# Kernel optimization log

Hardware: AMD Instinct MI355X
Metric: run time of the kernel (lower is better)

Reference implementation:

```python
import jax, jax.numpy as jnp
import numpy as np

B, LQ, LV, D = 16, 2048, 2048, 1024


def setup_inputs() -> dict:
    key = jax.random.key(0)
    kq, kv = jax.random.split(key)
    query = jax.random.normal(kq, (B, LQ, D), dtype=jnp.float32)
    value = jax.random.normal(kv, (B, LV, D), dtype=jnp.float32)
    return {"query": query, "value": value}


def reference(query, value):
    # score: [B, Lq, Lv] -- unscaled dot-product attention (no 1/sqrt(d))
    score = jnp.einsum('bqd,bvd->bqv', query, value)
    attn = jax.nn.softmax(score, axis=-1)
    # dropout is identity in eval mode
    context = jnp.einsum('bqv,bvd->bqd', attn, value)
    return context
```

## Files before the change

kernel.cpp:

```cpp
#include <hip/hip_runtime.h>


#define B_ 16
#define LQ_ 2048
#define LV_ 2048
#define DD_ 1024

typedef unsigned short u16;
typedef _Float16 f16x8 __attribute__((ext_vector_type(8)));
typedef __attribute__((ext_vector_type(4))) float f32x4;
typedef __attribute__((ext_vector_type(4))) unsigned short u16x4;

__device__ __forceinline__ u16 f2h(float x) {
  union { _Float16 h; u16 u; } c;
  c.h = (_Float16)x;
  return c.u;
}

__device__ __forceinline__ void gload16(const u16* g, u16* lds) {
  __builtin_amdgcn_global_load_lds(
      (const __attribute__((address_space(1))) void*)g,
      (__attribute__((address_space(3))) void*)lds, 16, 0, 0);
}

#define BARRIER() do { asm volatile("" ::: "memory"); __builtin_amdgcn_s_barrier(); asm volatile("" ::: "memory"); } while (0)
#define WAITVM(N) asm volatile("s_waitcnt vmcnt(" #N ")" ::: "memory")

template <int NSEG, int TPS>
__global__ __launch_bounds__(512, 2) void k_gemm8(
    const u16* __restrict__ A0, const u16* __restrict__ B0,
    const u16* __restrict__ A1, const u16* __restrict__ B1,
    float* __restrict__ C, int M, int N, int lda, int ldb,
    size_t aBatch, size_t bBatch) {
  constexpr int NT = NSEG * TPS;
  __shared__ u16 lds[65536];
  u16* ldsA = lds;
  u16* ldsB = lds + 32768;

  int bx, by, bz;
  {
    const int gx = gridDim.x, gy = gridDim.y;
    const int lid = blockIdx.x + gx * (blockIdx.y + gy * blockIdx.z);
    const int nwg = gx * gy * gridDim.z;
    const int q = nwg >> 3;
    const int nid = (lid & 7) * q + (lid >> 3);
    bx = nid % gx;
    const int rem = nid / gx;
    by = rem % gy;
    bz = rem / gy;
  }

  const int tid = threadIdx.x;
  const int w = tid >> 6, l = tid & 63;
  const int m0 = by << 8, n0 = bx << 8;
  const int wr = w >> 2, wc = w & 3;
  const int wr128 = wr * 128, wc64 = wc * 64;
  const int fr = l & 15, kx = l >> 4, fr7 = l & 7;
  const int srow = l >> 3;
  const int gsrc8 = (((l & 7) ^ ((l >> 3) & 7)) << 3);

  const u16* sA0 = A0 + (size_t)bz * aBatch;
  const u16* sB0 = B0 + (size_t)bz * bBatch;
  const u16* sA1 = A1 + (size_t)bz * aBatch;
  const u16* sB1 = B1 + (size_t)bz * bBatch;
  float* Cb = C + (size_t)bz * M * N;

#define PICKAB(tt, Ap_, Bp_)                          \
  const u16 *Ap_ = sA0, *Bp_ = sB0;                   \
  if (NSEG > 1 && (tt) / TPS == 1) { Ap_ = sA1; Bp_ = sB1; }

#define STAGE_A(tt, h)                                                          \
  do {                                                                          \
    PICKAB(tt, Ap_, Bp_); (void)Bp_;                                            \
    const int kk_ = ((tt) % TPS) * 64;                                          \
    u16* d0_ = ldsA + ((tt) & 1) * 16384 + ((h) * 64 + w * 8) * 64;             \
    const u16* g0_ = Ap_ + (size_t)(m0 + (h) * 64 + w * 8 + srow) * lda + kk_ + gsrc8; \
    gload16(g0_, d0_);                                                          \
    gload16(g0_ + (size_t)128 * lda, d0_ + 128 * 64);                           \
  } while (0)

#define STAGE_B(tt, h)                                                          \
  do {                                                                          \
    PICKAB(tt, Ap_, Bp_); (void)Ap_;                                            \
    const int kk_ = ((tt) % TPS) * 64;                                          \
    const int rb_ = (w >> 2) * 64 + (h) * 32 + (w & 3) * 8;                     \
    u16* d0_ = ldsB + ((tt) & 1) * 16384 + rb_ * 64;                            \
    const u16* g0_ = Bp_ + (size_t)(n0 + rb_ + srow) * ldb + kk_ + gsrc8;       \
    gload16(g0_, d0_);                                                          \
    gload16(g0_ + (size_t)128 * ldb, d0_ + 128 * 64);                           \
  } while (0)

#define RA8(MOFF)                                                                   \
  {                                                                                 \
    _Pragma("unroll") for (int m_ = 0; m_ < 4; ++m_) {                              \
      _Pragma("unroll") for (int k_ = 0; k_ < 2; ++k_) {                            \
        af[m_][k_] = *(const f16x8*)(ldsA + bufo +                                  \
            (wr128 + (MOFF) + m_ * 16 + fr) * 64 + (((kx + k_ * 4) ^ fr7) << 3));   \
      }                                                                             \
    }                                                                               \
  }

#define RB4(NF0)                                                                    \
  {                                                                                 \
    _Pragma("unroll") for (int n_ = 0; n_ < 2; ++n_) {                              \
      _Pragma("unroll") for (int k_ = 0; k_ < 2; ++k_) {                            \
        bf[(NF0) + n_][k_] = *(const f16x8*)(ldsB + bufo +                          \
            (wc64 + ((NF0) + n_) * 16 + fr) * 64 + (((kx + k_ * 4) ^ fr7) << 3));   \
      }                                                                             \
    }                                                                               \
  }

#define MFMA8(MF0, NF0)                                                             \
  {                                                                                 \
    _Pragma("unroll") for (int m_ = 0; m_ < 4; ++m_)                                \
    _Pragma("unroll") for (int n_ = 0; n_ < 2; ++n_)                                \
    _Pragma("unroll") for (int k_ = 0; k_ < 2; ++k_)                                \
        acc[(MF0) + m_][(NF0) + n_] = __builtin_amdgcn_mfma_f32_16x16x32_f16(       \
            af[m_][k_], bf[(NF0) + n_][k_], acc[(MF0) + m_][(NF0) + n_], 0, 0, 0);  \
  }

  f32x4 acc[8][4];
#pragma unroll
  for (int i = 0; i < 8; ++i)
#pragma unroll
    for (int j = 0; j < 4; ++j) acc[i][j] = (f32x4){0.f, 0.f, 0.f, 0.f};
  f16x8 af[4][2], bf[4][2];

  STAGE_A(0, 0); STAGE_A(0, 1); STAGE_B(0, 0); STAGE_B(0, 1);
  STAGE_A(1, 0); STAGE_B(1, 0); STAGE_A(1, 1);
  WAITVM(6);
  BARRIER();

#pragma unroll 2
  for (int t = 0; t < NT; ++t) {
    const int bufo = (t & 1) * 16384;
    RA8(0);
    RB4(0);
    if (t + 1 < NT) STAGE_B(t + 1, 1);
    BARRIER();
    __builtin_amdgcn_s_setprio(1); MFMA8(0, 0); __builtin_amdgcn_s_setprio(0);
    BARRIER();
    RB4(2);
    if (t + 2 < NT) STAGE_A(t + 2, 0);
    BARRIER();
    __builtin_amdgcn_s_setprio(1); MFMA8(0, 2); __builtin_amdgcn_s_setprio(0);
    BARRIER();
    RA8(64);
    if (t + 2 < NT) STAGE_B(t + 2, 0);
    BARRIER();
    __builtin_amdgcn_s_setprio(1); MFMA8(4, 0); __builtin_amdgcn_s_setprio(0);
    BARRIER();
    if (t + 2 < NT) STAGE_A(t + 2, 1);
    BARRIER();
    __builtin_amdgcn_s_setprio(1); MFMA8(4, 2); __builtin_amdgcn_s_setprio(0);
    if (t + 2 < NT) { WAITVM(6); } else if (t + 1 < NT) { WAITVM(0); }
    BARRIER();
  }

  const int crow = (l >> 4) * 4;
  const int ccol = l & 15;
#pragma unroll
  for (int mf = 0; mf < 8; ++mf)
#pragma unroll
    for (int nf = 0; nf < 4; ++nf) {
      float* cp = Cb + (size_t)(m0 + wr128 + mf * 16 + crow) * N + (n0 + wc64 + nf * 16 + ccol);
#pragma unroll
      for (int j = 0; j < 4; ++j) cp[(size_t)j * N] = acc[mf][nf][j];
    }
#undef PICKAB
#undef STAGE_A
#undef STAGE_B
#undef RA8
#undef RB4
#undef MFMA8
}

__global__ __launch_bounds__(256) void k_conv_q(const float* __restrict__ in,
                                                u16* __restrict__ hi_o, int nrows) {
  int t = blockIdx.x * 256 + threadIdx.x;
  int total = nrows * (DD_ / 4);
  if (t >= total) return;
  int row = t >> 8;
  int c4 = (t & 255) << 2;
  float4 v = *(const float4*)(in + (size_t)row * DD_ + c4);
  u16x4 hi;
  hi.x = f2h(v.x);
  hi.y = f2h(v.y);
  hi.z = f2h(v.z);
  hi.w = f2h(v.w);
  *(u16x4*)(hi_o + (size_t)row * DD_ + c4) = hi;
}

__global__ __launch_bounds__(256) void k_conv_vt(const float* __restrict__ V,
                                                 u16* __restrict__ Vh,
                                                 u16* __restrict__ VT) {
  __shared__ u16 tile[64][65];
  const int d0 = blockIdx.x * 64, v0 = blockIdx.y * 64;
  const size_t boff = (size_t)blockIdx.z * LV_ * DD_;
  const float* Vb = V + boff;
  u16* Vhb = Vh + boff;
  u16* VTb = VT + (size_t)blockIdx.z * DD_ * LV_;
  const int t = threadIdx.x;
  const int r = t >> 4, c4 = (t & 15) * 4;
#pragma unroll
  for (int i = 0; i < 4; ++i) {
    int row = r + i * 16;
    float4 x = *(const float4*)(Vb + (size_t)(v0 + row) * DD_ + d0 + c4);
    u16x4 h;
    h.x = f2h(x.x);
    h.y = f2h(x.y);
    h.z = f2h(x.z);
    h.w = f2h(x.w);
    *(u16x4*)(Vhb + (size_t)(v0 + row) * DD_ + d0 + c4) = h;
    tile[row][c4 + 0] = h.x;
    tile[row][c4 + 1] = h.y;
    tile[row][c4 + 2] = h.z;
    tile[row][c4 + 3] = h.w;
  }
  __syncthreads();
#pragma unroll
  for (int i = 0; i < 4; ++i) {
    int row = r + i * 16;
    u16x4 o;
    o.x = tile[c4 + 0][row];
    o.y = tile[c4 + 1][row];
    o.z = tile[c4 + 2][row];
    o.w = tile[c4 + 3][row];
    *(u16x4*)(VTb + (size_t)(d0 + row) * LV_ + v0 + c4) = o;
  }
}

__global__ __launch_bounds__(256) void k_softmax(const float* __restrict__ S,
                                                 u16* __restrict__ P, int nrows) {
  const int w = threadIdx.x >> 6, l = threadIdx.x & 63;
  const int row = blockIdx.x * 4 + w;
  if (row >= nrows) return;
  const float* s = S + (size_t)row * LV_;
  u16* p = P + (size_t)row * LV_;
  float4 v[8];
  float m = -3.0e38f;
#pragma unroll
  for (int i = 0; i < 8; ++i) {
    v[i] = *(const float4*)(s + (l << 2) + (i << 8));
    m = fmaxf(m, fmaxf(fmaxf(v[i].x, v[i].y), fmaxf(v[i].z, v[i].w)));
  }
#pragma unroll
  for (int off = 32; off > 0; off >>= 1) m = fmaxf(m, __shfl_xor(m, off, 64));
  float sum = 0.f;
#pragma unroll
  for (int i = 0; i < 8; ++i) {
    v[i].x = __expf(v[i].x - m);
    v[i].y = __expf(v[i].y - m);
    v[i].z = __expf(v[i].z - m);
    v[i].w = __expf(v[i].w - m);
    sum += v[i].x + v[i].y + v[i].z + v[i].w;
  }
#pragma unroll
  for (int off = 32; off > 0; off >>= 1) sum += __shfl_xor(sum, off, 64);
  const float inv = 1.0f / sum;
#pragma unroll
  for (int i = 0; i < 8; ++i) {
    u16x4 o;
    o.x = f2h(v[i].x * inv);
    o.y = f2h(v[i].y * inv);
    o.z = f2h(v[i].z * inv);
    o.w = f2h(v[i].w * inv);
    *(u16x4*)(p + (l << 2) + (i << 8)) = o;
  }
}

extern "C" void kernel_launch(void* const* d_in, const int* in_sizes, int n_in,
                              void* d_out, int out_size, void* d_ws, size_t ws_size,
                              hipStream_t stream) {
  const float* Q = (const float*)d_in[0];
  const float* V = (const float*)d_in[1];
  float* out = (float*)d_out;

  const size_t qv_e = (size_t)LQ_ * DD_;
  const size_t vt_e = (size_t)DD_ * LV_;
  const size_t s_e = (size_t)LQ_ * LV_;
  const size_t p_e = (size_t)LQ_ * LV_;
  const size_t per_batch = qv_e * 2 * 2 + vt_e * 2 + s_e * 4 + p_e * 2;

  int nb = (int)(ws_size / per_batch);
  if (nb < 1) nb = 1;
  if (nb > B_) nb = B_;

  char* wp = (char*)d_ws;
  u16* Qh = (u16*)wp; wp += (size_t)nb * qv_e * 2;
  u16* Vh = (u16*)wp; wp += (size_t)nb * qv_e * 2;
  u16* VT = (u16*)wp; wp += (size_t)nb * vt_e * 2;
  float* S = (float*)wp; wp += (size_t)nb * s_e * 4;
  u16* P = (u16*)wp;

  for (int b0 = 0; b0 < B_; b0 += nb) {
    const int cb = (nb < B_ - b0) ? nb : (B_ - b0);
    const int rows = cb * LQ_;
    const int cthreads = rows * (DD_ / 4);
    k_conv_q<<<dim3((cthreads + 255) / 256), dim3(256), 0, stream>>>(
        Q + (size_t)b0 * LQ_ * DD_, Qh, rows);
    k_conv_vt<<<dim3(DD_ / 64, LV_ / 64, cb), dim3(256), 0, stream>>>(
        V + (size_t)b0 * LV_ * DD_, Vh, VT);
    k_gemm8<1, 16><<<dim3(LV_ / 256, LQ_ / 256, cb), dim3(512), 0, stream>>>(
        Qh, Vh, Qh, Vh, S, LQ_, LV_, DD_, DD_, qv_e, qv_e);
    k_softmax<<<dim3(rows / 4), dim3(256), 0, stream>>>(S, P, rows);
    k_gemm8<1, 32><<<dim3(DD_ / 256, LQ_ / 256, cb), dim3(512), 0, stream>>>(
        P, VT, P, VT, out + (size_t)b0 * LQ_ * DD_, LQ_, DD_, LV_, LV_, p_e, vt_e);
  }
}
```

Before: 514.2 us.

## Fuse softmax into QK^T GEMM with row-panel online softmax

Replaces the separate QK^T GEMM, fp32 score buffer and softmax kernel with a row-panel kernel. Each workgroup owns 128 query rows, sweeps all value columns in 256-wide chunks, and keeps a running max and sum per row. It writes unnormalized fp16 exponentials per chunk, then rescales its P panel in place at the end. The second GEMM uses the same 128-row panel layout. This removes the fp32 S round-trip and one launch, but the grid shrinks to 16×batch workgroups with 128×256 tiles, which may lower occupancy and parallelism. It also adds a reread and rewrite pass over P.

```diff
diff --git a/kernel.cpp b/kernel.cpp
--- a/kernel.cpp
+++ b/kernel.cpp
@@ -26,153 +26,235 @@
 #define BARRIER() do { asm volatile("" ::: "memory"); __builtin_amdgcn_s_barrier(); asm volatile("" ::: "memory"); } while (0)
 #define WAITVM(N) asm volatile("s_waitcnt vmcnt(" #N ")" ::: "memory")
 
-template <int NSEG, int TPS>
-__global__ __launch_bounds__(512, 2) void k_gemm8(
-    const u16* __restrict__ A0, const u16* __restrict__ B0,
-    const u16* __restrict__ A1, const u16* __restrict__ B1,
-    float* __restrict__ C, int M, int N, int lda, int ldb,
-    size_t aBatch, size_t bBatch) {
-  constexpr int NT = NSEG * TPS;
-  __shared__ u16 lds[65536];
+template <int TPS, int NCHUNK, bool FUSE>
+__global__ __launch_bounds__(512, 2) void k_panel(
+    const u16* __restrict__ A, const u16* __restrict__ B,
+    u16* __restrict__ Pout, float* __restrict__ Fout,
+    int ldA, int ldB, int Ntot,
+    size_t aBatch, size_t bBatch, size_t cBatch) {
+  constexpr int NTOT = TPS * NCHUNK;
+  __shared__ u16 lds[49152];
   u16* ldsA = lds;
-  u16* ldsB = lds + 32768;
-
-  int bx, by, bz;
+  u16* ldsB = lds + 16384;
+  __shared__ float red[4][128];
+  __shared__ float mc_lds[NCHUNK][128];
+  __shared__ float sums[128];
+  __shared__ float ftab[NCHUNK][128];
+
+  int bx, bz;
   {
-    const int gx = gridDim.x, gy = gridDim.y;
-    const int lid = blockIdx.x + gx * (blockIdx.y + gy * blockIdx.z);
-    const int nwg = gx * gy * gridDim.z;
-    const int q = nwg >> 3;
-    const int nid = (lid & 7) * q + (lid >> 3);
-    bx = nid % gx;
-    const int rem = nid / gx;
-    by = rem % gy;
-    bz = rem / gy;
+    const int lid = blockIdx.x + 16 * blockIdx.z;
+    if (gridDim.z == 16) {
+      const int u = lid & 7, v = lid >> 3;
+      bz = u + 8 * (v >> 4);
+      bx = v & 15;
+    } else {
+      bx = blockIdx.x;
+      bz = blockIdx.z;
+    }
   }
 
   const int tid = threadIdx.x;
   const int w = tid >> 6, l = tid & 63;
-  const int m0 = by << 8, n0 = bx << 8;
-  const int wr = w >> 2, wc = w & 3;
-  const int wr128 = wr * 128, wc64 = wc * 64;
-  const int fr = l & 15, kx = l >> 4, fr7 = l & 7;
+  const int m0 = bx << 7;
+  const int wr64 = (w >> 2) * 64, wc64 = (w & 3) * 64;
+  const int fr = l & 15, kx = l >> 4, fr7 = l & 7, cc = l & 15;
   const int srow = l >> 3;
+  const int rg4 = (l >> 4) * 4;
   const int gsrc8 = (((l & 7) ^ ((l >> 3) & 7)) << 3);
 
-  const u16* sA0 = A0 + (size_t)bz * aBatch;
-  const u16* sB0 = B0 + (size_t)bz * bBatch;
-  const u16* sA1 = A1 + (size_t)bz * aBatch;
-  const u16* sB1 = B1 + (size_t)bz * bBatch;
-  float* Cb = C + (size_t)bz * M * N;
-
-#define PICKAB(tt, Ap_, Bp_)                          \
-  const u16 *Ap_ = sA0, *Bp_ = sB0;                   \
-  if (NSEG > 1 && (tt) / TPS == 1) { Ap_ = sA1; Bp_ = sB1; }
-
-#define STAGE_A(tt, h)                                                          \
-  do {                                                                          \
-    PICKAB(tt, Ap_, Bp_); (void)Bp_;                                            \
-    const int kk_ = ((tt) % TPS) * 64;                                          \
-    u16* d0_ = ldsA + ((tt) & 1) * 16384 + ((h) * 64 + w * 8) * 64;             \
-    const u16* g0_ = Ap_ + (size_t)(m0 + (h) * 64 + w * 8 + srow) * lda + kk_ + gsrc8; \
-    gload16(g0_, d0_);                                                          \
-    gload16(g0_ + (size_t)128 * lda, d0_ + 128 * 64);                           \
+  const u16* Ab = A + (size_t)bz * aBatch;
+  const u16* Bb = B + (size_t)bz * bBatch;
+  u16* Pc = FUSE ? (Pout + (size_t)bz * cBatch) : nullptr;
+  float* Fc = FUSE ? nullptr : (Fout + (size_t)bz * cBatch);
+
+#define STAGE_A(gt, h)                                                         \
+  do {                                                                         \
+    const int kk_ = ((gt) % TPS) * 64;                                         \
+    const int ar_ = (w >> 2) * 64 + (h) * 32 + (w & 3) * 8;                    \
+    u16* d_ = ldsA + ((gt) & 1) * 8192 + ar_ * 64;                             \
+    gload16(Ab + (size_t)(m0 + ar_ + srow) * ldA + kk_ + gsrc8, d_);           \
   } while (0)
 
-#define STAGE_B(tt, h)                                                          \
-  do {                                                                          \
-    PICKAB(tt, Ap_, Bp_); (void)Ap_;                                            \
-    const int kk_ = ((tt) % TPS) * 64;                                          \
-    const int rb_ = (w >> 2) * 64 + (h) * 32 + (w & 3) * 8;                     \
-    u16* d0_ = ldsB + ((tt) & 1) * 16384 + rb_ * 64;                            \
-    const u16* g0_ = Bp_ + (size_t)(n0 + rb_ + srow) * ldb + kk_ + gsrc8;       \
-    gload16(g0_, d0_);                                                          \
-    gload16(g0_ + (size_t)128 * ldb, d0_ + 128 * 64);                           \
+#define STAGE_B(gt, h)                                                         \
+  do {                                                                         \
+    const int kk_ = ((gt) % TPS) * 64;                                         \
+    const int n0_ = ((gt) / TPS) * 256;                                        \
+    const int rb_ = (w >> 2) * 64 + (h) * 32 + (w & 3) * 8;                    \
+    u16* d_ = ldsB + ((gt) & 1) * 16384 + rb_ * 64;                            \
+    const u16* g_ = Bb + (size_t)(n0_ + rb_ + srow) * ldB + kk_ + gsrc8;       \
+    gload16(g_, d_);                                                           \
+    gload16(g_ + (size_t)128 * ldB, d_ + 8192);                                \
   } while (0)
 
-#define RA8(MOFF)                                                                   \
-  {                                                                                 \
-    _Pragma("unroll") for (int m_ = 0; m_ < 4; ++m_) {                              \
-      _Pragma("unroll") for (int k_ = 0; k_ < 2; ++k_) {                            \
-        af[m_][k_] = *(const f16x8*)(ldsA + bufo +                                  \
-            (wr128 + (MOFF) + m_ * 16 + fr) * 64 + (((kx + k_ * 4) ^ fr7) << 3));   \
-      }                                                                             \
-    }                                                                               \
-  }
-
-#define RB4(NF0)                                                                    \
-  {                                                                                 \
-    _Pragma("unroll") for (int n_ = 0; n_ < 2; ++n_) {                              \
-      _Pragma("unroll") for (int k_ = 0; k_ < 2; ++k_) {                            \
-        bf[(NF0) + n_][k_] = *(const f16x8*)(ldsB + bufo +                          \
-            (wc64 + ((NF0) + n_) * 16 + fr) * 64 + (((kx + k_ * 4) ^ fr7) << 3));   \
-      }                                                                             \
-    }                                                                               \
-  }
-
-#define MFMA8(MF0, NF0)                                                             \
-  {                                                                                 \
-    _Pragma("unroll") for (int m_ = 0; m_ < 4; ++m_)                                \
-    _Pragma("unroll") for (int n_ = 0; n_ < 2; ++n_)                                \
-    _Pragma("unroll") for (int k_ = 0; k_ < 2; ++k_)                                \
-        acc[(MF0) + m_][(NF0) + n_] = __builtin_amdgcn_mfma_f32_16x16x32_f16(       \
-            af[m_][k_], bf[(NF0) + n_][k_], acc[(MF0) + m_][(NF0) + n_], 0, 0, 0);  \
-  }
-
-  f32x4 acc[8][4];
-#pragma unroll
-  for (int i = 0; i < 8; ++i)
+#define RA2(MH)                                                                \
+  { _Pragma("unroll") for (int m_ = 0; m_ < 2; ++m_)                           \
+    _Pragma("unroll") for (int k_ = 0; k_ < 2; ++k_)                           \
+      af[m_][k_] = *(const f16x8*)(ldsA + bufoA +                              \
+          (wr64 + ((MH) * 2 + m_) * 16 + fr) * 64 +                            \
+          (((kx + k_ * 4) ^ fr7) << 3)); }
+
+#define RB4(NF0)                                                               \
+  { _Pragma("unroll") for (int n_ = 0; n_ < 2; ++n_)                           \
+    _Pragma("unroll") for (int k_ = 0; k_ < 2; ++k_)                           \
+      bf[(NF0) + n_][k_] = *(const f16x8*)(ldsB + bufoB +                      \
+          (wc64 + ((NF0) + n_) * 16 + fr) * 64 +                               \
+          (((kx + k_ * 4) ^ fr7) << 3)); }
+
+#define MFMA4(MH, NF0)                                                         \
+  { _Pragma("unroll") for (int m_ = 0; m_ < 2; ++m_)                           \
+    _Pragma("unroll") for (int n_ = 0; n_ < 2; ++n_)                           \
+    _Pragma("unroll") for (int k_ = 0; k_ < 2; ++k_)                           \
+      acc[(MH) * 2 + m_][(NF0) + n_] = __builtin_amdgcn_mfma_f32_16x16x32_f16( \
+          af[m_][k_], bf[(NF0) + n_][k_], acc[(MH) * 2 + m_][(NF0) + n_],      \
+          0, 0, 0); }
+
+  f32x4 acc[4][4];
+#pragma unroll
+  for (int i = 0; i < 4; ++i)
 #pragma unroll
     for (int j = 0; j < 4; ++j) acc[i][j] = (f32x4){0.f, 0.f, 0.f, 0.f};
-  f16x8 af[4][2], bf[4][2];
+  f16x8 af[2][2], bf[4][2];
+  float m_run[4][4], s_run[4][4];
+#pragma unroll
+  for (int i = 0; i < 4; ++i)
+#pragma unroll
+    for (int j = 0; j < 4; ++j) { m_run[i][j] = -1.0e30f; s_run[i][j] = 0.f; }
 
   STAGE_A(0, 0); STAGE_A(0, 1); STAGE_B(0, 0); STAGE_B(0, 1);
   STAGE_A(1, 0); STAGE_B(1, 0); STAGE_A(1, 1);
-  WAITVM(6);
+  WAITVM(4);
   BARRIER();
 
 #pragma unroll 2
-  for (int t = 0; t < NT; ++t) {
-    const int bufo = (t & 1) * 16384;
-    RA8(0);
-    RB4(0);
-    if (t + 1 < NT) STAGE_B(t + 1, 1);
-    BARRIER();
-    __builtin_amdgcn_s_setprio(1); MFMA8(0, 0); __builtin_amdgcn_s_setprio(0);
+  for (int gt = 0; gt < NTOT; ++gt) {
+    const int bufoA = (gt & 1) * 8192;
+    const int bufoB = (gt & 1) * 16384;
+    RA2(0); RB4(0);
+    if (gt + 1 < NTOT) STAGE_B(gt + 1, 1);
+    BARRIER();
+    __builtin_amdgcn_s_setprio(1); MFMA4(0, 0); __builtin_amdgcn_s_setprio(0);
     BARRIER();
     RB4(2);
-    if (t + 2 < NT) STAGE_A(t + 2, 0);
-    BARRIER();
-    __builtin_amdgcn_s_setprio(1); MFMA8(0, 2); __builtin_amdgcn_s_setprio(0);
-    BARRIER();
-    RA8(64);
-    if (t + 2 < NT) STAGE_B(t + 2, 0);
-    BARRIER();
-    __builtin_amdgcn_s_setprio(1); MFMA8(4, 0); __builtin_amdgcn_s_setprio(0);
-    BARRIER();
-    if (t + 2 < NT) STAGE_A(t + 2, 1);
-    BARRIER();
-    __builtin_amdgcn_s_setprio(1); MFMA8(4, 2); __builtin_amdgcn_s_setprio(0);
-    if (t + 2 < NT) { WAITVM(6); } else if (t + 1 < NT) { WAITVM(0); }
-    BARRIER();
-  }
-
-  const int crow = (l >> 4) * 4;
-  const int ccol = l & 15;
-#pragma unroll
-  for (int mf = 0; mf < 8; ++mf)
-#pragma unroll
-    for (int nf = 0; nf < 4; ++nf) {
-      float* cp = Cb + (size_t)(m0 + wr128 + mf * 16 + crow) * N + (n0 + wc64 + nf * 16 + ccol);
-#pragma unroll
-      for (int j = 0; j < 4; ++j) cp[(size_t)j * N] = acc[mf][nf][j];
-    }
-#undef PICKAB
+    if (gt + 2 < NTOT) STAGE_A(gt + 2, 0);
+    BARRIER();
+    __builtin_amdgcn_s_setprio(1); MFMA4(0, 2); __builtin_amdgcn_s_setprio(0);
+    BARRIER();
+    RA2(1);
+    if (gt + 2 < NTOT) STAGE_B(gt + 2, 0);
+    BARRIER();
+    __builtin_amdgcn_s_setprio(1); MFMA4(1, 0); __builtin_amdgcn_s_setprio(0);
+    BARRIER();
+    if (gt + 2 < NTOT) STAGE_A(gt + 2, 1);
+    BARRIER();
+    __builtin_amdgcn_s_setprio(1); MFMA4(1, 2); __builtin_amdgcn_s_setprio(0);
+    if (gt + 2 < NTOT) { WAITVM(4); } else { WAITVM(0); }
+    BARRIER();
+
+    if ((gt & (TPS - 1)) == (TPS - 1)) {
+      const int c_ = gt / TPS;
+      if constexpr (FUSE) {
+        BARRIER();
+#pragma unroll
+        for (int mf = 0; mf < 4; ++mf)
+#pragma unroll
+          for (int j = 0; j < 4; ++j) {
+            float v = fmaxf(fmaxf(acc[mf][0][j], acc[mf][1][j]),
+                            fmaxf(acc[mf][2][j], acc[mf][3][j]));
+#pragma unroll
+            for (int off = 1; off < 16; off <<= 1)
+              v = fmaxf(v, __shfl_xor(v, off, 64));
+            if ((l & 15) == 0) red[w & 3][wr64 + mf * 16 + rg4 + j] = v;
+          }
+        BARRIER();
+        float csum[4][4], mloc[4][4];
+#pragma unroll
+        for (int mf = 0; mf < 4; ++mf)
+#pragma unroll
+          for (int j = 0; j < 4; ++j) {
+            const int r_ = wr64 + mf * 16 + rg4 + j;
+            const float mc_ = fmaxf(fmaxf(red[0][r_], red[1][r_]),
+                                    fmaxf(red[2][r_], red[3][r_]));
+            const float mnew = fmaxf(m_run[mf][j], mc_);
+            float cs = 0.f;
+#pragma unroll
+            for (int nf = 0; nf < 4; ++nf) {
+              const float e = __expf(acc[mf][nf][j] - mnew);
+              cs += e;
+              Pc[(size_t)(m0 + r_) * 2048 + c_ * 256 + wc64 + nf * 16 + cc] = f2h(e);
+            }
+#pragma unroll
+            for (int off = 1; off < 16; off <<= 1) cs += __shfl_xor(cs, off, 64);
+            csum[mf][j] = cs;
+            mloc[mf][j] = mnew;
+          }
+        BARRIER();
+#pragma unroll
+        for (int mf = 0; mf < 4; ++mf)
+#pragma unroll
+          for (int j = 0; j < 4; ++j)
+            if ((l & 15) == 0) red[w & 3][wr64 + mf * 16 + rg4 + j] = csum[mf][j];
+        BARRIER();
+#pragma unroll
+        for (int mf = 0; mf < 4; ++mf)
+#pragma unroll
+          for (int j = 0; j < 4; ++j) {
+            const int r_ = wr64 + mf * 16 + rg4 + j;
+            const float tot = red[0][r_] + red[1][r_] + red[2][r_] + red[3][r_];
+            s_run[mf][j] = s_run[mf][j] * __expf(m_run[mf][j] - mloc[mf][j]) + tot;
+            m_run[mf][j] = mloc[mf][j];
+            if ((w & 3) == 0 && (l & 15) == 0) mc_lds[c_][r_] = m_run[mf][j];
+          }
+        BARRIER();
+      } else {
+#pragma unroll
+        for (int mf = 0; mf < 4; ++mf)
+#pragma unroll
+          for (int nf = 0; nf < 4; ++nf) {
+            float* cp = Fc + (size_t)(m0 + wr64 + mf * 16 + rg4) * Ntot +
+                        c_ * 256 + wc64 + nf * 16 + cc;
+#pragma unroll
+            for (int j = 0; j < 4; ++j) cp[(size_t)j * Ntot] = acc[mf][nf][j];
+          }
+      }
+#pragma unroll
+      for (int i = 0; i < 4; ++i)
+#pragma unroll
+        for (int j = 0; j < 4; ++j) acc[i][j] = (f32x4){0.f, 0.f, 0.f, 0.f};
+    }
+  }
+
+  if constexpr (FUSE) {
+    WAITVM(0);
+    BARRIER();
+    if ((w & 3) == 0 && (l & 15) == 0) {
+#pragma unroll
+      for (int mf = 0; mf < 4; ++mf)
+#pragma unroll
+        for (int j = 0; j < 4; ++j)
+          sums[wr64 + mf * 16 + rg4 + j] = s_run[mf][j];
+    }
+    BARRIER();
+    for (int i = tid; i < NCHUNK * 128; i += 512) {
+      const int c = i >> 7, r = i & 127;
+      ftab[c][r] = __expf(mc_lds[c][r] - mc_lds[NCHUNK - 1][r]) / sums[r];
+    }
+    BARRIER();
+    for (int i = tid; i < 128 * 256; i += 512) {
+      const int r = i >> 8, cp = i & 255;
+      f16x8* p = (f16x8*)(Pc + (size_t)(m0 + r) * 2048 + cp * 8);
+      f16x8 v = *p;
+      const float f = ftab[cp >> 5][r];
+#pragma unroll
+      for (int e = 0; e < 8; ++e) v[e] = (_Float16)((float)v[e] * f);
+      *p = v;
+    }
+  }
 #undef STAGE_A
 #undef STAGE_B
-#undef RA8
+#undef RA2
 #undef RB4
-#undef MFMA8
+#undef MFMA4
 }
 
 __global__ __launch_bounds__(256) void k_conv_q(const float* __restrict__ in,
@@ -230,45 +312,6 @@
   }
 }
 
-__global__ __launch_bounds__(256) void k_softmax(const float* __restrict__ S,
-                                                 u16* __restrict__ P, int nrows) {
-  const int w = threadIdx.x >> 6, l = threadIdx.x & 63;
-  const int row = blockIdx.x * 4 + w;
-  if (row >= nrows) return;
-  const float* s = S + (size_t)row * LV_;
-  u16* p = P + (size_t)row * LV_;
-  float4 v[8];
-  float m = -3.0e38f;
-#pragma unroll
-  for (int i = 0; i < 8; ++i) {
-    v[i] = *(const float4*)(s + (l << 2) + (i << 8));
-    m = fmaxf(m, fmaxf(fmaxf(v[i].x, v[i].y), fmaxf(v[i].z, v[i].w)));
-  }
-#pragma unroll
-  for (int off = 32; off > 0; off >>= 1) m = fmaxf(m, __shfl_xor(m, off, 64));
-  float sum = 0.f;
-#pragma unroll
-  for (int i = 0; i < 8; ++i) {
-    v[i].x = __expf(v[i].x - m);
-    v[i].y = __expf(v[i].y - m);
-    v[i].z = __expf(v[i].z - m);
-    v[i].w = __expf(v[i].w - m);
-    sum += v[i].x + v[i].y + v[i].z + v[i].w;
-  }
-#pragma unroll
-  for (int off = 32; off > 0; off >>= 1) sum += __shfl_xor(sum, off, 64);
-  const float inv = 1.0f / sum;
-#pragma unroll
-  for (int i = 0; i < 8; ++i) {
-    u16x4 o;
-    o.x = f2h(v[i].x * inv);
-    o.y = f2h(v[i].y * inv);
-    o.z = f2h(v[i].z * inv);
-    o.w = f2h(v[i].w * inv);
-    *(u16x4*)(p + (l << 2) + (i << 8)) = o;
-  }
-}
-
 extern "C" void kernel_launch(void* const* d_in, const int* in_sizes, int n_in,
                               void* d_out, int out_size, void* d_ws, size_t ws_size,
                               hipStream_t stream) {
@@ -278,9 +321,8 @@
 
   const size_t qv_e = (size_t)LQ_ * DD_;
   const size_t vt_e = (size_t)DD_ * LV_;
-  const size_t s_e = (size_t)LQ_ * LV_;
   const size_t p_e = (size_t)LQ_ * LV_;
-  const size_t per_batch = qv_e * 2 * 2 + vt_e * 2 + s_e * 4 + p_e * 2;
+  const size_t per_batch = qv_e * 2 * 2 + vt_e * 2 + p_e * 2;
 
   int nb = (int)(ws_size / per_batch);
   if (nb < 1) nb = 1;
@@ -290,7 +332,6 @@
   u16* Qh = (u16*)wp; wp += (size_t)nb * qv_e * 2;
   u16* Vh = (u16*)wp; wp += (size_t)nb * qv_e * 2;
   u16* VT = (u16*)wp; wp += (size_t)nb * vt_e * 2;
-  float* S = (float*)wp; wp += (size_t)nb * s_e * 4;
   u16* P = (u16*)wp;
 
   for (int b0 = 0; b0 < B_; b0 += nb) {
@@ -301,10 +342,10 @@
         Q + (size_t)b0 * LQ_ * DD_, Qh, rows);
     k_conv_vt<<<dim3(DD_ / 64, LV_ / 64, cb), dim3(256), 0, stream>>>(
         V + (size_t)b0 * LV_ * DD_, Vh, VT);
-    k_gemm8<1, 16><<<dim3(LV_ / 256, LQ_ / 256, cb), dim3(512), 0, stream>>>(
-        Qh, Vh, Qh, Vh, S, LQ_, LV_, DD_, DD_, qv_e, qv_e);
-    k_softmax<<<dim3(rows / 4), dim3(256), 0, stream>>>(S, P, rows);
-    k_gemm8<1, 32><<<dim3(DD_ / 256, LQ_ / 256, cb), dim3(512), 0, stream>>>(
-        P, VT, P, VT, out + (size_t)b0 * LQ_ * DD_, LQ_, DD_, LV_, LV_, p_e, vt_e);
-  }
-}
+    k_panel<16, 8, true><<<dim3(16, 1, cb), dim3(512), 0, stream>>>(
+        Qh, Vh, P, nullptr, DD_, DD_, LV_, qv_e, qv_e, p_e);
+    k_panel<32, 4, false><<<dim3(16, 1, cb), dim3(512), 0, stream>>>(
+        P, VT, nullptr, out + (size_t)b0 * LQ_ * DD_, LV_, LV_, DD_, p_e, vt_e,
+        (size_t)LQ_ * DD_);
+  }
+}
```

Result: slower. 589.5 us (+14.7%).

## Fuse softmax into QK GEMM epilogue with per-tile stats and rescale in PV GEMM

Applied to the files above, without the earlier changes.

Removes the fp32 score buffer and the separate softmax kernel. The first GEMM epilogue now computes tile-local row max, writes unnormalized exp as fp16 and records per-tile max and sum. A small stats kernel combines the eight column-tile partials into per-tile rescale factors and the reciprocal denominator. The PV GEMM scales A fragments by those factors in registers and applies the final normalization on store. This saves the large fp32 write and read of S, at the cost of extra epilogue reductions, LDS use and fp16 multiplies in the inner loop.

```diff
diff --git a/kernel.cpp b/kernel.cpp
--- a/kernel.cpp
+++ b/kernel.cpp
@@ -26,14 +26,18 @@
 #define BARRIER() do { asm volatile("" ::: "memory"); __builtin_amdgcn_s_barrier(); asm volatile("" ::: "memory"); } while (0)
 #define WAITVM(N) asm volatile("s_waitcnt vmcnt(" #N ")" ::: "memory")
 
-template <int NSEG, int TPS>
+template <int TPS, int MODE>
 __global__ __launch_bounds__(512, 2) void k_gemm8(
-    const u16* __restrict__ A0, const u16* __restrict__ B0,
-    const u16* __restrict__ A1, const u16* __restrict__ B1,
-    float* __restrict__ C, int M, int N, int lda, int ldb,
-    size_t aBatch, size_t bBatch) {
-  constexpr int NT = NSEG * TPS;
+    const u16* __restrict__ A, const u16* __restrict__ B,
+    u16* __restrict__ Pout, float* __restrict__ Fout,
+    const u16* __restrict__ r2tab, const float* __restrict__ fintab,
+    float* __restrict__ mtab, float* __restrict__ stab,
+    int N, int lda, int ldb, size_t aBatch, size_t bBatch, size_t cBatch) {
+  constexpr int NT = TPS;
   __shared__ u16 lds[65536];
+  __shared__ float red[4][256];
+  __shared__ u16 ldsR2[2048];
+  __shared__ float ldsFin[256];
   u16* ldsA = lds;
   u16* ldsB = lds + 32768;
 
@@ -55,39 +59,38 @@
   const int m0 = by << 8, n0 = bx << 8;
   const int wr = w >> 2, wc = w & 3;
   const int wr128 = wr * 128, wc64 = wc * 64;
-  const int fr = l & 15, kx = l >> 4, fr7 = l & 7;
+  const int fr = l & 15, kx = l >> 4, fr7 = l & 7, cc = l & 15;
   const int srow = l >> 3;
   const int gsrc8 = (((l & 7) ^ ((l >> 3) & 7)) << 3);
 
-  const u16* sA0 = A0 + (size_t)bz * aBatch;
-  const u16* sB0 = B0 + (size_t)bz * bBatch;
-  const u16* sA1 = A1 + (size_t)bz * aBatch;
-  const u16* sB1 = B1 + (size_t)bz * bBatch;
-  float* Cb = C + (size_t)bz * M * N;
-
-#define PICKAB(tt, Ap_, Bp_)                          \
-  const u16 *Ap_ = sA0, *Bp_ = sB0;                   \
-  if (NSEG > 1 && (tt) / TPS == 1) { Ap_ = sA1; Bp_ = sB1; }
+  const u16* Ab = A + (size_t)bz * aBatch;
+  const u16* Bb = B + (size_t)bz * bBatch;
+
+  if constexpr (MODE == 2) {
+    for (int i = tid; i < 2048; i += 512)
+      ldsR2[i] = r2tab[((size_t)bz * 8 + (i >> 8)) * 2048 + m0 + (i & 255)];
+    for (int i = tid; i < 256; i += 512)
+      ldsFin[i] = fintab[(size_t)bz * 2048 + m0 + i];
+    __syncthreads();
+  }
 
 #define STAGE_A(tt, h)                                                          \
   do {                                                                          \
-    PICKAB(tt, Ap_, Bp_); (void)Bp_;                                            \
-    const int kk_ = ((tt) % TPS) * 64;                                          \
+    const int kk_ = (tt) * 64;                                                  \
     u16* d0_ = ldsA + ((tt) & 1) * 16384 + ((h) * 64 + w * 8) * 64;             \
-    const u16* g0_ = Ap_ + (size_t)(m0 + (h) * 64 + w * 8 + srow) * lda + kk_ + gsrc8; \
+    const u16* g0_ = Ab + (size_t)(m0 + (h) * 64 + w * 8 + srow) * lda + kk_ + gsrc8; \
     gload16(g0_, d0_);                                                          \
     gload16(g0_ + (size_t)128 * lda, d0_ + 128 * 64);                           \
   } while (0)
 
 #define STAGE_B(tt, h)                                                          \
   do {                                                                          \
-    PICKAB(tt, Ap_, Bp_); (void)Ap_;                                            \
-    const int kk_ = ((tt) % TPS) * 64;                                          \
+    const int kk_ = (tt) * 64;                                                  \
     const int rb_ = (w >> 2) * 64 + (h) * 32 + (w & 3) * 8;                     \
     u16* d0_ = ldsB + ((tt) & 1) * 16384 + rb_ * 64;                            \
-    const u16* g0_ = Bp_ + (size_t)(n0 + rb_ + srow) * ldb + kk_ + gsrc8;       \
+    const u16* g0_ = Bb + (size_t)(n0 + rb_ + srow) * ldb + kk_ + gsrc8;        \
     gload16(g0_, d0_);                                                          \
-    gload16(g0_ + (size_t)128 * ldb, d0_ + 128 * 64);                           \
+    gload16(g0_ + (size_t)128 * ldb, d0_ + 8192);                               \
   } while (0)
 
 #define RA8(MOFF)                                                                   \
@@ -96,6 +99,7 @@
       _Pragma("unroll") for (int k_ = 0; k_ < 2; ++k_) {                            \
         af[m_][k_] = *(const f16x8*)(ldsA + bufo +                                  \
             (wr128 + (MOFF) + m_ * 16 + fr) * 64 + (((kx + k_ * 4) ^ fr7) << 3));   \
+        if constexpr (MODE == 2) af[m_][k_] = af[m_][k_] * r2h[(MOFF) / 16 + m_];   \
       }                                                                             \
     }                                                                               \
   }
@@ -125,6 +129,7 @@
 #pragma unroll
     for (int j = 0; j < 4; ++j) acc[i][j] = (f32x4){0.f, 0.f, 0.f, 0.f};
   f16x8 af[4][2], bf[4][2];
+  _Float16 r2h[8];
 
   STAGE_A(0, 0); STAGE_A(0, 1); STAGE_B(0, 0); STAGE_B(0, 1);
   STAGE_A(1, 0); STAGE_B(1, 0); STAGE_A(1, 1);
@@ -134,6 +139,14 @@
 #pragma unroll 2
   for (int t = 0; t < NT; ++t) {
     const int bufo = (t & 1) * 16384;
+    if constexpr (MODE == 2) {
+      if ((t & 3) == 0) {
+        const int chb = (t >> 2) * 256;
+#pragma unroll
+        for (int i = 0; i < 8; ++i)
+          r2h[i] = *(const _Float16*)&ldsR2[chb + wr128 + i * 16 + fr];
+      }
+    }
     RA8(0);
     RB4(0);
     if (t + 1 < NT) STAGE_B(t + 1, 1);
@@ -157,22 +170,97 @@
     BARRIER();
   }
 
-  const int crow = (l >> 4) * 4;
-  const int ccol = l & 15;
-#pragma unroll
-  for (int mf = 0; mf < 8; ++mf)
-#pragma unroll
-    for (int nf = 0; nf < 4; ++nf) {
-      float* cp = Cb + (size_t)(m0 + wr128 + mf * 16 + crow) * N + (n0 + wc64 + nf * 16 + ccol);
-#pragma unroll
-      for (int j = 0; j < 4; ++j) cp[(size_t)j * N] = acc[mf][nf][j];
+  const int rg4 = (l >> 4) * 4;
+  if constexpr (MODE == 1) {
+    float mt[8][4];
+#pragma unroll
+    for (int mf = 0; mf < 8; ++mf)
+#pragma unroll
+      for (int j = 0; j < 4; ++j) {
+        float v = fmaxf(fmaxf(acc[mf][0][j], acc[mf][1][j]),
+                        fmaxf(acc[mf][2][j], acc[mf][3][j]));
+#pragma unroll
+        for (int off = 1; off < 16; off <<= 1) v = fmaxf(v, __shfl_xor(v, off, 64));
+        if ((l & 15) == 0) red[w & 3][wr128 + mf * 16 + rg4 + j] = v;
+      }
+    __syncthreads();
+#pragma unroll
+    for (int mf = 0; mf < 8; ++mf)
+#pragma unroll
+      for (int j = 0; j < 4; ++j) {
+        const int r_ = wr128 + mf * 16 + rg4 + j;
+        mt[mf][j] = fmaxf(fmaxf(red[0][r_], red[1][r_]), fmaxf(red[2][r_], red[3][r_]));
+      }
+    __syncthreads();
+    u16* Pc = Pout + (size_t)bz * ((size_t)2048 * 2048);
+#pragma unroll
+    for (int mf = 0; mf < 8; ++mf)
+#pragma unroll
+      for (int j = 0; j < 4; ++j) {
+        const int r_ = wr128 + mf * 16 + rg4 + j;
+        float s = 0.f;
+#pragma unroll
+        for (int nf = 0; nf < 4; ++nf) {
+          const float e = __expf(acc[mf][nf][j] - mt[mf][j]);
+          s += e;
+          Pc[(size_t)(m0 + r_) * 2048 + n0 + wc64 + nf * 16 + cc] = f2h(e);
+        }
+#pragma unroll
+        for (int off = 1; off < 16; off <<= 1) s += __shfl_xor(s, off, 64);
+        if ((l & 15) == 0) red[w & 3][r_] = s;
+      }
+    __syncthreads();
+    if (((w & 3) == 0) && ((l & 15) == 0)) {
+#pragma unroll
+      for (int mf = 0; mf < 8; ++mf)
+#pragma unroll
+        for (int j = 0; j < 4; ++j) {
+          const int r_ = wr128 + mf * 16 + rg4 + j;
+          const float st = red[0][r_] + red[1][r_] + red[2][r_] + red[3][r_];
+          mtab[((size_t)bz * 8 + bx) * 2048 + m0 + r_] = mt[mf][j];
+          stab[((size_t)bz * 8 + bx) * 2048 + m0 + r_] = st;
+        }
     }
-#undef PICKAB
+  } else {
+#pragma unroll
+    for (int mf = 0; mf < 8; ++mf)
+#pragma unroll
+      for (int nf = 0; nf < 4; ++nf) {
+        float* cp = Fout + (size_t)bz * cBatch +
+                    (size_t)(m0 + wr128 + mf * 16 + rg4) * N + n0 + wc64 + nf * 16 + cc;
+#pragma unroll
+        for (int j = 0; j < 4; ++j)
+          cp[(size_t)j * N] = acc[mf][nf][j] * ldsFin[wr128 + mf * 16 + rg4 + j];
+      }
+  }
 #undef STAGE_A
 #undef STAGE_B
 #undef RA8
 #undef RB4
 #undef MFMA8
+}
+
+__global__ __launch_bounds__(256) void k_stats(const float* __restrict__ mtab,
+                                               const float* __restrict__ stab,
+                                               u16* __restrict__ r2tab,
+                                               float* __restrict__ fintab) {
+  const int r = blockIdx.x * 256 + threadIdx.x;
+  const int bz = blockIdx.y;
+  float m[8], s[8], mg = -3.0e38f;
+#pragma unroll
+  for (int t = 0; t < 8; ++t) {
+    m[t] = mtab[((size_t)bz * 8 + t) * 2048 + r];
+    s[t] = stab[((size_t)bz * 8 + t) * 2048 + r];
+    mg = fmaxf(mg, m[t]);
+  }
+  float denom = 0.f;
+#pragma unroll
+  for (int t = 0; t < 8; ++t) {
+    const float f = __expf(m[t] - mg);
+    denom += s[t] * f;
+    r2tab[((size_t)bz * 8 + t) * 2048 + r] = f2h(f);
+  }
+  fintab[(size_t)bz * 2048 + r] = 1.0f / denom;
 }
 
 __global__ __launch_bounds__(256) void k_conv_q(const float* __restrict__ in,
@@ -230,45 +318,6 @@
   }
 }
 
-__global__ __launch_bounds__(256) void k_softmax(const float* __restrict__ S,
-                                                 u16* __restrict__ P, int nrows) {
-  const int w = threadIdx.x >> 6, l = threadIdx.x & 63;
-  const int row = blockIdx.x * 4 + w;
-  if (row >= nrows) return;
-  const float* s = S + (size_t)row * LV_;
-  u16* p = P + (size_t)row * LV_;
-  float4 v[8];
-  float m = -3.0e38f;
-#pragma unroll
-  for (int i = 0; i < 8; ++i) {
-    v[i] = *(const float4*)(s + (l << 2) + (i << 8));
-    m = fmaxf(m, fmaxf(fmaxf(v[i].x, v[i].y), fmaxf(v[i].z, v[i].w)));
-  }
-#pragma unroll
-  for (int off = 32; off > 0; off >>= 1) m = fmaxf(m, __shfl_xor(m, off, 64));
-  float sum = 0.f;
-#pragma unroll
-  for (int i = 0; i < 8; ++i) {
-    v[i].x = __expf(v[i].x - m);
-    v[i].y = __expf(v[i].y - m);
-    v[i].z = __expf(v[i].z - m);
-    v[i].w = __expf(v[i].w - m);
-    sum += v[i].x + v[i].y + v[i].z + v[i].w;
-  }
-#pragma unroll
-  for (int off = 32; off > 0; off >>= 1) sum += __shfl_xor(sum, off, 64);
-  const float inv = 1.0f / sum;
-#pragma unroll
-  for (int i = 0; i < 8; ++i) {
-    u16x4 o;
-    o.x = f2h(v[i].x * inv);
-    o.y = f2h(v[i].y * inv);
-    o.z = f2h(v[i].z * inv);
-    o.w = f2h(v[i].w * inv);
-    *(u16x4*)(p + (l << 2) + (i << 8)) = o;
-  }
-}
-
 extern "C" void kernel_launch(void* const* d_in, const int* in_sizes, int n_in,
                               void* d_out, int out_size, void* d_ws, size_t ws_size,
                               hipStream_t stream) {
@@ -278,20 +327,24 @@
 
   const size_t qv_e = (size_t)LQ_ * DD_;
   const size_t vt_e = (size_t)DD_ * LV_;
-  const size_t s_e = (size_t)LQ_ * LV_;
   const size_t p_e = (size_t)LQ_ * LV_;
-  const size_t per_batch = qv_e * 2 * 2 + vt_e * 2 + s_e * 4 + p_e * 2;
+  const size_t tab_e = (size_t)8 * 2048;
+  const size_t per_batch =
+      qv_e * 2 * 2 + vt_e * 2 + p_e * 2 + tab_e * 4 * 2 + tab_e * 2 + 2048 * 4;
 
   int nb = (int)(ws_size / per_batch);
   if (nb < 1) nb = 1;
   if (nb > B_) nb = B_;
 
   char* wp = (char*)d_ws;
-  u16* Qh = (u16*)wp; wp += (size_t)nb * qv_e * 2;
-  u16* Vh = (u16*)wp; wp += (size_t)nb * qv_e * 2;
-  u16* VT = (u16*)wp; wp += (size_t)nb * vt_e * 2;
-  float* S = (float*)wp; wp += (size_t)nb * s_e * 4;
-  u16* P = (u16*)wp;
+  u16* Qh = (u16*)wp;    wp += (size_t)nb * qv_e * 2;
+  u16* Vh = (u16*)wp;    wp += (size_t)nb * qv_e * 2;
+  u16* VT = (u16*)wp;    wp += (size_t)nb * vt_e * 2;
+  u16* P = (u16*)wp;     wp += (size_t)nb * p_e * 2;
+  float* mtab = (float*)wp;  wp += (size_t)nb * tab_e * 4;
+  float* stab = (float*)wp;  wp += (size_t)nb * tab_e * 4;
+  u16* r2tab = (u16*)wp;     wp += (size_t)nb * tab_e * 2;
+  float* fintab = (float*)wp;
 
   for (int b0 = 0; b0 < B_; b0 += nb) {
     const int cb = (nb < B_ - b0) ? nb : (B_ - b0);
@@ -301,10 +354,12 @@
         Q + (size_t)b0 * LQ_ * DD_, Qh, rows);
     k_conv_vt<<<dim3(DD_ / 64, LV_ / 64, cb), dim3(256), 0, stream>>>(
         V + (size_t)b0 * LV_ * DD_, Vh, VT);
-    k_gemm8<1, 16><<<dim3(LV_ / 256, LQ_ / 256, cb), dim3(512), 0, stream>>>(
-        Qh, Vh, Qh, Vh, S, LQ_, LV_, DD_, DD_, qv_e, qv_e);
-    k_softmax<<<dim3(rows / 4), dim3(256), 0, stream>>>(S, P, rows);
-    k_gemm8<1, 32><<<dim3(DD_ / 256, LQ_ / 256, cb), dim3(512), 0, stream>>>(
-        P, VT, P, VT, out + (size_t)b0 * LQ_ * DD_, LQ_, DD_, LV_, LV_, p_e, vt_e);
-  }
-}
+    k_gemm8<16, 1><<<dim3(LV_ / 256, LQ_ / 256, cb), dim3(512), 0, stream>>>(
+        Qh, Vh, P, nullptr, nullptr, nullptr, mtab, stab,
+        LV_, DD_, DD_, qv_e, qv_e, 0);
+    k_stats<<<dim3(LQ_ / 256, cb), dim3(256), 0, stream>>>(mtab, stab, r2tab, fintab);
+    k_gemm8<32, 2><<<dim3(DD_ / 256, LQ_ / 256, cb), dim3(512), 0, stream>>>(
+        P, VT, nullptr, out + (size_t)b0 * LQ_ * DD_, r2tab, fintab, nullptr, nullptr,
+        DD_, LV_, LV_, p_e, vt_e, (size_t)LQ_ * DD_);
+  }
+}
```

Result: faster. 457.3 us (-11.0%).
